# Performance work log

Hardware: AMD Instinct MI355X
Metric: run time of the kernel (lower is better)

Reference implementation:

```python
import jax, jax.numpy as jnp
import numpy as np

N, E, C_IN, C_OUT, K, D_D = 50000, 800000, 16, 64, 3, 7


def setup_inputs() -> dict:
    key = jax.random.key(0)
    ks = jax.random.split(key, 10)
    s = 0.05
    x = jax.random.normal(ks[0], (N, C_IN), jnp.float32)
    edge_index = jax.random.randint(ks[1], (2, E), 0, N, dtype=jnp.int64)
    edge_weight = jax.random.uniform(ks[2], (E,), jnp.float32)
    h0 = jax.random.normal(ks[3], (N, C_OUT), jnp.float32)
    # stacked ChebConv params: gate order [z, r, h]
    Wx = jax.random.normal(ks[4], (3, K, C_IN, C_OUT), jnp.float32) * s
    Wh = jax.random.normal(ks[5], (3, K, C_OUT, C_OUT), jnp.float32) * s
    bx = jax.random.normal(ks[6], (3, C_OUT), jnp.float32) * s
    bh = jax.random.normal(ks[7], (3, C_OUT), jnp.float32) * s
    Wlin = jax.random.normal(ks[8], (C_OUT, D_D), jnp.float32) * s
    blin = jax.random.normal(ks[9], (D_D,), jnp.float32) * s
    return dict(x=x, edge_index=edge_index, edge_weight=edge_weight, h0=h0,
                Wx=Wx, Wh=Wh, bx=bx, bh=bh, Wlin=Wlin, blin=blin)


def _norm(src, dst, edge_weight, n):
    # ChebConv sym normalization with lambda_max=2:
    # L_sym = I - D^-1/2 A D^-1/2;  L_tilde = 2L/lambda_max - I = -D^-1/2 A D^-1/2
    w = jnp.where(src == dst, 0.0, edge_weight)  # remove self loops
    deg = jax.ops.segment_sum(w, src, num_segments=n)
    dinv = jnp.where(deg > 0, 1.0 / jnp.sqrt(deg), 0.0)
    return -dinv[src] * w * dinv[dst]


def _cheb(t, W, b, src, dst, nw, n):
    # K-hop Chebyshev recursion: Tx_{k+1} = 2*L~*Tx_k - Tx_{k-1}
    prop = lambda v: jax.ops.segment_sum(nw[:, None] * v[src], dst, num_segments=n)
    Tx0 = t
    out = Tx0 @ W[0]
    Tx1 = prop(Tx0)
    out = out + Tx1 @ W[1]
    for k in range(2, W.shape[0]):
        Tx2 = 2.0 * prop(Tx1) - Tx0
        out = out + Tx2 @ W[k]
        Tx0, Tx1 = Tx1, Tx2
    return out + b


def reference(x, edge_index, edge_weight, h0, Wx, Wh, bx, bh, Wlin, blin):
    n = x.shape[0]
    src, dst = edge_index[0], edge_index[1]
    nw = _norm(src, dst, edge_weight, n)
    z = jax.nn.sigmoid(_cheb(x, Wx[0], bx[0], src, dst, nw, n)
                       + _cheb(h0, Wh[0], bh[0], src, dst, nw, n))
    r = jax.nn.sigmoid(_cheb(x, Wx[1], bx[1], src, dst, nw, n)
                       + _cheb(h0, Wh[1], bh[1], src, dst, nw, n))
    htil = jnp.tanh(_cheb(x, Wx[2], bx[2], src, dst, nw, n)
                    + _cheb(h0 * r, Wh[2], bh[2], src, dst, nw, n))
    h = z * h0 + (1.0 - z) * htil
    y = jax.nn.relu(h) @ Wlin + blin
    return (jax.lax.stop_gradient(h), y)
```

## Files before the change

kernel.cpp:

```cpp
#include <hip/hip_runtime.h>

constexpr int NN = 50000;
constexpr int NE = 800000;
constexpr int CI = 16;
constexpr int CO = 64;
constexpr int DD = 7;

constexpr int NBUCK = 196;
constexpr int EPB   = 4096;
constexpr int NBLK3 = (NE + EPB - 1) / EPB;
constexpr int TBL   = NBUCK * NBLK3;

typedef __bf16 bf16x8 __attribute__((ext_vector_type(8)));
typedef float  f32x4  __attribute__((ext_vector_type(4)));
typedef float  f32x2  __attribute__((ext_vector_type(2)));

__device__ inline float blo(unsigned u) { return __uint_as_float(u << 16); }
__device__ inline float bhi(unsigned u) { return __uint_as_float(u & 0xffff0000u); }

__device__ inline void acc8_fp8(float acc[8], float w, uint2 u) {
    f32x2 c;
    c = __builtin_amdgcn_cvt_pk_f32_fp8(u.x, false); acc[0] += w * c[0]; acc[1] += w * c[1];
    c = __builtin_amdgcn_cvt_pk_f32_fp8(u.x, true);  acc[2] += w * c[0]; acc[3] += w * c[1];
    c = __builtin_amdgcn_cvt_pk_f32_fp8(u.y, false); acc[4] += w * c[0]; acc[5] += w * c[1];
    c = __builtin_amdgcn_cvt_pk_f32_fp8(u.y, true);  acc[6] += w * c[0]; acc[7] += w * c[1];
}
__device__ inline uint2 pack_fp8x8(const float o[8]) {
    int t0 = __builtin_amdgcn_cvt_pk_fp8_f32(o[0], o[1], 0, false);
    t0 = __builtin_amdgcn_cvt_pk_fp8_f32(o[2], o[3], t0, true);
    int t1 = __builtin_amdgcn_cvt_pk_fp8_f32(o[4], o[5], 0, false);
    t1 = __builtin_amdgcn_cvt_pk_fp8_f32(o[6], o[7], t1, true);
    uint2 r; r.x = (unsigned)t0; r.y = (unsigned)t1; return r;
}
__device__ inline unsigned char fp8_of(float v) {
    return (unsigned char)(__builtin_amdgcn_cvt_pk_fp8_f32(v, v, 0, false) & 0xff);
}


constexpr int XOCT = NN * CI / 8;
constexpr int HOCT = NN * CO / 8;
constexpr int CB = (XOCT + HOCT + 255) / 256;

__global__ void __launch_bounds__(256) k_count(
    const int* __restrict__ src, const int* __restrict__ dst,
    int* __restrict__ Cd, int* __restrict__ Cs,
    const float* __restrict__ x, const float* __restrict__ h0,
    __bf16* __restrict__ x_bf, __bf16* __restrict__ h0_bf, unsigned char* __restrict__ h0_f8,
    const float* __restrict__ Wx, const float* __restrict__ Wh,
    const float* __restrict__ bx, const float* __restrict__ bh,
    bf16x8* __restrict__ BfragZR, bf16x8* __restrict__ BfragHT, float* __restrict__ biasC) {
    int b = blockIdx.x;
    if (b < NBLK3) {
        __shared__ int hd[NBUCK], hs[NBUCK];
        for (int i = threadIdx.x; i < NBUCK; i += 256) { hd[i] = 0; hs[i] = 0; }
        __syncthreads();
        int base = b * EPB;
#pragma unroll
        for (int k = 0; k < EPB / 256; k++) {
            int e = base + k * 256 + threadIdx.x;
            if (e < NE) {
                int s = src[e], d = dst[e];
                atomicAdd(&hd[d >> 8], 1);
                atomicAdd(&hs[s >> 8], 1);
            }
        }
        __syncthreads();
        for (int i = threadIdx.x; i < NBUCK; i += 256) {
            Cd[i * NBLK3 + b] = hd[i];
            Cs[i * NBLK3 + b] = hs[i];
        }
    } else if (b < NBLK3 + CB) {
        int t = (b - NBLK3) * 256 + threadIdx.x;
        if (t < XOCT) {
            const float* sp = x + (size_t)t * 8;
            float4 a = *(const float4*)sp;
            float4 c = *(const float4*)(sp + 4);
            bf16x8 o;
            o[0] = (__bf16)a.x; o[1] = (__bf16)a.y; o[2] = (__bf16)a.z; o[3] = (__bf16)a.w;
            o[4] = (__bf16)c.x; o[5] = (__bf16)c.y; o[6] = (__bf16)c.z; o[7] = (__bf16)c.w;
            *(bf16x8*)(x_bf + (size_t)t * 8) = o;
        } else if (t < XOCT + HOCT) {
            int u = t - XOCT;
            const float* sp = h0 + (size_t)u * 8;
            float4 a = *(const float4*)sp;
            float4 c = *(const float4*)(sp + 4);
            bf16x8 o;
            o[0] = (__bf16)a.x; o[1] = (__bf16)a.y; o[2] = (__bf16)a.z; o[3] = (__bf16)a.w;
            o[4] = (__bf16)c.x; o[5] = (__bf16)c.y; o[6] = (__bf16)c.z; o[7] = (__bf16)c.w;
            *(bf16x8*)(h0_bf + (size_t)u * 8) = o;
            float f[8] = {a.x, a.y, a.z, a.w, c.x, c.y, c.z, c.w};
            *(uint2*)(h0_f8 + (size_t)u * 8) = pack_fp8x8(f);
        }
    } else {
        int tid = (b - NBLK3 - CB) * 256 + threadIdx.x;
        if (tid < 6144) {
            int e = tid, gate, n, kk, l;
            if (e < 4096) {
                int t = e >> 9, rem = e & 511;
                kk = rem >> 6; l = rem & 63;
                n = t * 16 + (l & 15);
                gate = n >> 6;
            } else {
                int e2 = e - 4096;
                int t = e2 >> 9, rem = e2 & 511;
                kk = rem >> 6; l = rem & 63;
                n = t * 16 + (l & 15);
                gate = 2;
            }
            int co = n & 63;
            int k0 = kk * 32 + (l >> 4) * 8;
            bf16x8 f;
#pragma unroll
            for (int j = 0; j < 8; j++) {
                int k = k0 + j;
                float w = 0.f;
                if (k < 48) {
                    int kb = k >> 4, ci = k & 15;
                    const float* Wg = Wx + gate * 3 * 16 * 64;
                    float w0 = Wg[(kb * 16 + ci) * 64 + co];
                    if (kb == 0)      w = w0 - Wg[(2 * 16 + ci) * 64 + co];
                    else if (kb == 1) w = w0;
                    else              w = 2.f * w0;
                } else if (k < 240) {
                    int kh = k - 48, kb = kh >> 6, ci = kh & 63;
                    const float* Wg = Wh + gate * 3 * 64 * 64;
                    float w0 = Wg[(kb * 64 + ci) * 64 + co];
                    if (kb == 0)      w = w0 - Wg[(2 * 64 + ci) * 64 + co];
                    else if (kb == 1) w = w0;
                    else              w = 2.f * w0;
                }
                f[j] = (__bf16)w;
            }
            if (e < 4096) BfragZR[e] = f; else BfragHT[e - 4096] = f;
        } else if (tid < 6144 + 192) {
            int i = tid - 6144;
            biasC[i] = bx[i] + bh[i];
        }
    }
}


__global__ void __launch_bounds__(1024) k_scan_tables(int* __restrict__ Cd, int* __restrict__ Cs) {
    int* C = (blockIdx.x == 0) ? Cd : Cs;
    constexpr int CHUNK = (TBL + 1023) / 1024;
    __shared__ int part[1024];
    int t = threadIdx.x;
    int base = t * CHUNK;
    int v[CHUNK];
    int s = 0;
#pragma unroll
    for (int j = 0; j < CHUNK; j++) {
        int idx = base + j;
        int xv = (idx < TBL) ? C[idx] : 0;
        v[j] = s;
        s += xv;
    }
    part[t] = s;
    __syncthreads();
    for (int off = 1; off < 1024; off <<= 1) {
        int p = (t >= off) ? part[t - off] : 0;
        __syncthreads();
        part[t] += p;
        __syncthreads();
    }
    int tb = (t > 0) ? part[t - 1] : 0;
#pragma unroll
    for (int j = 0; j < CHUNK; j++) {
        int idx = base + j;
        if (idx < TBL) C[idx] = tb + v[j];
    }
}


__global__ void __launch_bounds__(256) k_scatter(
    const int* __restrict__ src, const int* __restrict__ dst, const float* __restrict__ ew,
    const int* __restrict__ Cd, const int* __restrict__ Cs,
    uint2* __restrict__ drec, unsigned* __restrict__ srec) {
    __shared__ int cd[NBUCK], cs[NBUCK];
    int b = blockIdx.x;
    for (int i = threadIdx.x; i < NBUCK; i += 256) {
        cd[i] = Cd[i * NBLK3 + b];
        cs[i] = Cs[i * NBLK3 + b];
    }
    __syncthreads();
    int base = b * EPB;
#pragma unroll
    for (int k = 0; k < EPB / 256; k++) {
        int e = base + k * 256 + threadIdx.x;
        if (e < NE) {
            int s = src[e], d = dst[e];
            float w = (s == d) ? 0.f : ew[e];
            __bf16 wb = (__bf16)w;
            unsigned wu = (unsigned)__builtin_bit_cast(unsigned short, wb);
            int pd = atomicAdd(&cd[d >> 8], 1);
            drec[pd] = make_uint2((unsigned)s | (wu << 16), (unsigned)(d & 255));
            int ps = atomicAdd(&cs[s >> 8], 1);
            srec[ps] = (__builtin_bit_cast(unsigned, w) & 0xFFFFFF00u) | (unsigned)(s & 255);
        }
    }
}


__global__ void __launch_bounds__(256) k_dinv(
    const int* __restrict__ Cs, const unsigned* __restrict__ srec, float* __restrict__ dinv) {
    int bkt = blockIdx.x;
    __shared__ float acc[256];
    acc[threadIdx.x] = 0.f;
    __syncthreads();
    int beg = Cs[bkt * NBLK3];
    int end = (bkt == NBUCK - 1) ? NE : Cs[(bkt + 1) * NBLK3];
    for (int i = beg + threadIdx.x; i < end; i += 256) {
        unsigned r = srec[i];
        atomicAdd(&acc[r & 255], __uint_as_float(r & 0xFFFFFF00u));
    }
    __syncthreads();
    int node = bkt * 256 + threadIdx.x;
    if (node < NN) {
        float dsum = acc[threadIdx.x];
        dinv[node] = (dsum > 0.f) ? (1.f / sqrtf(dsum)) : 0.f;
    }
}


__global__ void __launch_bounds__(256) k_build(
    const int* __restrict__ Cd, const uint2* __restrict__ drec, const float* __restrict__ dinv,
    int* __restrict__ rowptr, unsigned* __restrict__ csr_ew) {
    int bkt = blockIdx.x;
    __shared__ int cnt[256], sc[256], cur[256];
    int t = threadIdx.x;
    cnt[t] = 0;
    __syncthreads();
    int beg = Cd[bkt * NBLK3];
    int end = (bkt == NBUCK - 1) ? NE : Cd[(bkt + 1) * NBLK3];
    for (int i = beg + t; i < end; i += 256) atomicAdd(&cnt[drec[i].y], 1);
    __syncthreads();
    int val = cnt[t];
    sc[t] = val;
    __syncthreads();
    for (int off = 1; off < 256; off <<= 1) {
        int p = (t >= off) ? sc[t - off] : 0;
        __syncthreads();
        sc[t] += p;
        __syncthreads();
    }
    int ex = sc[t] - val;
    int node = bkt * 256 + t;
    if (node <= NN) rowptr[node] = beg + ex;
    cur[t] = ex;
    __syncthreads();
    for (int i = beg + t; i < end; i += 256) {
        uint2 r = drec[i];
        int slot = beg + atomicAdd(&cur[r.y], 1);
        unsigned s = r.x & 0xffff;
        float w = bhi(r.x);
        float wp = dinv[s] * w;
        __bf16 wb = (__bf16)wp;
        unsigned ub = (unsigned)__builtin_bit_cast(unsigned short, wb);
        csr_ew[slot] = s | (ub << 16);
    }
}


__device__ inline void fprop_body(int n, int lane,
                                  const unsigned char* __restrict__ vh8,
                                  const __bf16* __restrict__ vx,
                                  const float* __restrict__ dinv,
                                  const int* __restrict__ rowptr,
                                  const unsigned* __restrict__ ew,
                                  __bf16* __restrict__ outh_bf,
                                  unsigned char* __restrict__ outh_f8,
                                  __bf16* __restrict__ outx) {
    int j = lane >> 3, cg = lane & 7;
    int beg = rowptr[n], end = rowptr[n + 1];
    float f = -dinv[n];
    unsigned pmeta = (beg + lane < end) ? ew[beg + lane] : 0u;
    int deg = end - beg;
    int nIt = (deg >= 64) ? 8 : ((deg + 7) >> 3);
    float acc[8] = {0.f, 0.f, 0.f, 0.f, 0.f, 0.f, 0.f, 0.f};
    float ax0 = 0.f, ax1 = 0.f;
#pragma unroll
    for (int t = 0; t < 8; t++) {
// ... 69 lines not shown
        unsigned p = ew[e];
        float w = bhi(p);
        int s = p & 0xffff;
        uint2 u = *(const uint2*)(v8 + (size_t)s * 64 + cg * 8);
        acc8_fp8(acc, w, u);
    }
#pragma unroll
    for (int m = 8; m <= 32; m <<= 1) {
#pragma unroll
        for (int i = 0; i < 8; i++) acc[i] += __shfl_xor(acc[i], m, 64);
    }
    if (lane < 8) {
        float o[8];
#pragma unroll
        for (int i = 0; i < 8; i++) o[i] = f * acc[i];
        bf16x8 st;
#pragma unroll
        for (int i = 0; i < 8; i++) st[i] = (__bf16)o[i];
        *(bf16x8*)(out_bf + (size_t)n * 64 + lane * 8) = st;
        if (out_f8) *(uint2*)(out_f8 + (size_t)n * 64 + lane * 8) = pack_fp8x8(o);
    }
}

__global__ void __launch_bounds__(256) k_fprop(
    const unsigned char* __restrict__ vh8, const __bf16* __restrict__ vx,
    const float* __restrict__ dinv,
    const int* __restrict__ rowptr, const unsigned* __restrict__ ew,
    __bf16* __restrict__ outh_bf, unsigned char* __restrict__ outh_f8,
    __bf16* __restrict__ outx) {
    int n = blockIdx.x * 4 + (threadIdx.x >> 6);
    if (n >= NN) return;
    fprop_body(n, threadIdx.x & 63, vh8, vx, dinv, rowptr, ew, outh_bf, outh_f8, outx);
}

__global__ void __launch_bounds__(256) k_prop64(
    const unsigned char* __restrict__ v8, const float* __restrict__ dinv,
    const int* __restrict__ rowptr, const unsigned* __restrict__ ew,
    __bf16* __restrict__ out_bf, unsigned char* __restrict__ out_f8) {
    int n = blockIdx.x * 4 + (threadIdx.x >> 6);
    if (n >= NN) return;
    prop64_body(n, threadIdx.x & 63, v8, dinv, rowptr, ew, out_bf, out_f8);
}


__device__ inline bf16x8 load_a_bf(int c, int m,
                                   const __bf16* __restrict__ xb, const __bf16* __restrict__ t1,
                                   const __bf16* __restrict__ t2, const __bf16* __restrict__ hb,
                                   const __bf16* __restrict__ h1, const __bf16* __restrict__ h2) {
    if (c >= 30) {
        bf16x8 a;
#pragma unroll
        for (int j = 0; j < 8; j++) a[j] = (__bf16)0.f;
        return a;
    }
    if (c < 6) {
        const __bf16* base = (c < 2) ? xb : ((c < 4) ? t1 : t2);
        return *(const bf16x8*)(base + (size_t)m * 16 + (c & 1) * 8);
    }
    int d = c - 6;
    const __bf16* base = (d < 8) ? hb : ((d < 16) ? h1 : h2);
    return *(const bf16x8*)(base + (size_t)m * 64 + (d & 7) * 8);
}

__global__ void __launch_bounds__(256) k_mfma_zr(
    const __bf16* __restrict__ xb, const __bf16* __restrict__ t1, const __bf16* __restrict__ t2,
    const __bf16* __restrict__ hb, const __bf16* __restrict__ h1, const __bf16* __restrict__ h2,
    const bf16x8* __restrict__ Bfrag, const float* __restrict__ biasC,
    __bf16* __restrict__ z_bf, __bf16* __restrict__ hr_bf, unsigned char* __restrict__ hr_f8) {
    int wv = (blockIdx.x * 256 + threadIdx.x) >> 6;
    if (wv >= NN / 16) return;
    int lane = threadIdx.x & 63;
    int q = lane >> 4, r16 = lane & 15;
    int ma = wv * 16 + r16;
    f32x4 acc[8];
#pragma unroll
    for (int t = 0; t < 8; t++) acc[t] = (f32x4){0.f, 0.f, 0.f, 0.f};
#pragma unroll
    for (int kk = 0; kk < 8; kk++) {
        bf16x8 a = load_a_bf(kk * 4 + q, ma, xb, t1, t2, hb, h1, h2);
#pragma unroll
        for (int t = 0; t < 8; t++)
            acc[t] = __builtin_amdgcn_mfma_f32_16x16x32_bf16(a, Bfrag[(t * 8 + kk) * 64 + lane], acc[t], 0, 0, 0);
    }
    int mbase = wv * 16 + q * 4;
#pragma unroll
    for (int t = 0; t < 8; t++) {
        int co = t * 16 + r16;
        float bias = biasC[co];
        int col = co & 63;
#pragma unroll
        for (int reg = 0; reg < 4; reg++) {
            int mm = mbase + reg;
            float p = acc[t][reg] + bias;
            float s = 1.f / (1.f + __expf(-p));
            if (t < 4) z_bf[(size_t)mm * 64 + col] = (__bf16)s;
            else {
                float hrv = s * (float)hb[(size_t)mm * 64 + col];
                hr_bf[(size_t)mm * 64 + col] = (__bf16)hrv;
                hr_f8[(size_t)mm * 64 + col] = fp8_of(hrv);
            }
        }
    }
}

__global__ void __launch_bounds__(256) k_mfma_ht(
    const __bf16* __restrict__ xb, const __bf16* __restrict__ t1, const __bf16* __restrict__ t2,
    const __bf16* __restrict__ hrb, const __bf16* __restrict__ r1, const __bf16* __restrict__ r2,
    const bf16x8* __restrict__ Bfrag, const float* __restrict__ biasC,
    const __bf16* __restrict__ z_bf, const float* __restrict__ h0,
    const float* __restrict__ Wlin, const float* __restrict__ blin,
    float* __restrict__ hout, float* __restrict__ yout) {
    int wv = (blockIdx.x * 256 + threadIdx.x) >> 6;
    if (wv >= NN / 16) return;
    int lane = threadIdx.x & 63;
    int q = lane >> 4, r16 = lane & 15;
    int ma = wv * 16 + r16;
    f32x4 acc[4];
#pragma unroll
    for (int t = 0; t < 4; t++) acc[t] = (f32x4){0.f, 0.f, 0.f, 0.f};
#pragma unroll
    for (int kk = 0; kk < 8; kk++) {
        bf16x8 a = load_a_bf(kk * 4 + q, ma, xb, t1, t2, hrb, r1, r2);
#pragma unroll
        for (int t = 0; t < 4; t++)
            acc[t] = __builtin_amdgcn_mfma_f32_16x16x32_bf16(a, Bfrag[(t * 8 + kk) * 64 + lane], acc[t], 0, 0, 0);
    }
    int mbase = wv * 16 + q * 4;
    float hbuf[4][4];
#pragma unroll
    for (int t = 0; t < 4; t++) {
        int co = t * 16 + r16;
        float bias = biasC[128 + co];
#pragma unroll
        for (int reg = 0; reg < 4; reg++) {
            int mm = mbase + reg;
            float p = acc[t][reg] + bias;
            float htl = tanhf(p);
            float zv = (float)z_bf[(size_t)mm * 64 + co];
            float h0v = h0[(size_t)mm * 64 + co];
            float hn = zv * h0v + (1.f - zv) * htl;
            hout[(size_t)mm * 64 + co] = hn;
            hbuf[t][reg] = hn;
        }
    }
    float ya[4][DD];
#pragma unroll
    for (int reg = 0; reg < 4; reg++)
#pragma unroll
        for (int d = 0; d < DD; d++) ya[reg][d] = 0.f;
#pragma unroll
    for (int t = 0; t < 4; t++) {
        int cb = (t * 16 + r16) * DD;
        float wl[DD];
#pragma unroll
        for (int d = 0; d < DD; d++) wl[d] = Wlin[cb + d];
#pragma unroll
        for (int reg = 0; reg < 4; reg++) {
            float rh = fmaxf(hbuf[t][reg], 0.f);
#pragma unroll
            for (int d = 0; d < DD; d++) ya[reg][d] += rh * wl[d];
        }
    }
#pragma unroll
    for (int m = 1; m <= 8; m <<= 1) {
#pragma unroll
        for (int reg = 0; reg < 4; reg++)
#pragma unroll
            for (int d = 0; d < DD; d++) ya[reg][d] += __shfl_xor(ya[reg][d], m, 64);
    }
    if (r16 < DD) {
        float b = blin[r16];
#pragma unroll
        for (int reg = 0; reg < 4; reg++) {
            float v = (r16 == 0) ? ya[reg][0] : (r16 == 1) ? ya[reg][1] : (r16 == 2) ? ya[reg][2]
                    : (r16 == 3) ? ya[reg][3] : (r16 == 4) ? ya[reg][4] : (r16 == 5) ? ya[reg][5]
                    : ya[reg][6];
            yout[(size_t)(mbase + reg) * DD + r16] = v + b;
        }
    }
}


extern "C" void kernel_launch(void* const* d_in, const int* in_sizes, int n_in,
                              void* d_out, int out_size, void* d_ws, size_t ws_size,
                              hipStream_t stream) {
    (void)in_sizes; (void)n_in; (void)out_size; (void)ws_size;
    const float* x    = (const float*)d_in[0];
    const int*   eidx = (const int*)d_in[1];
    const float* ew   = (const float*)d_in[2];
    const float* h0   = (const float*)d_in[3];
    const float* Wx   = (const float*)d_in[4];
    const float* Wh   = (const float*)d_in[5];
    const float* bx   = (const float*)d_in[6];
    const float* bh   = (const float*)d_in[7];
    const float* Wlin = (const float*)d_in[8];
    const float* blin = (const float*)d_in[9];
    const int* src = eidx;
    const int* dst = eidx + NE;

    char* ws = (char*)d_ws;
    size_t off = 0;
    auto alloc = [&](size_t nbytes) -> void* {
        void* p = ws + off;
        off += (nbytes + 255) & ~(size_t)255;
        return p;
    };
    int*    Cd      = (int*)alloc((size_t)TBL * 4);
    int*    Cs      = (int*)alloc((size_t)TBL * 4);
    uint2*  drec    = (uint2*)alloc((size_t)NE * 8);
    unsigned* srec  = (unsigned*)alloc((size_t)NE * 4);
    float*  dinv    = (float*)alloc(NN * 4);
    int*    rowptr  = (int*)alloc((NN + 1) * 4);
    unsigned* csr_ew = (unsigned*)alloc((size_t)NE * 4);
    __bf16* x_bf    = (__bf16*)alloc((size_t)NN * CI * 2);
    __bf16* h0_bf   = (__bf16*)alloc((size_t)NN * CO * 2);
    unsigned char* h0_f8 = (unsigned char*)alloc((size_t)NN * CO);
    unsigned char* T1_f8 = (unsigned char*)alloc((size_t)NN * CO);
    unsigned char* hr_f8 = (unsigned char*)alloc((size_t)NN * CO);
    __bf16* Tx1     = (__bf16*)alloc((size_t)NN * CI * 2);
    __bf16* Tx2     = (__bf16*)alloc((size_t)NN * CI * 2);
    __bf16* Th1     = (__bf16*)alloc((size_t)NN * CO * 2);
    __bf16* Th2     = (__bf16*)alloc((size_t)NN * CO * 2);
    __bf16* hr_bf   = (__bf16*)alloc((size_t)NN * CO * 2);
    __bf16* z_bf    = (__bf16*)alloc((size_t)NN * CO * 2);
    bf16x8* BfragZR = (bf16x8*)alloc(4096 * 16);
    bf16x8* BfragHT = (bf16x8*)alloc(2048 * 16);
    float*  biasC   = (float*)alloc(192 * 4);

    float* hout = (float*)d_out;
    float* yout = hout + (size_t)NN * CO;

    const int PROPB = (NN + 3) / 4;
    const int GEMMB = (NN / 16 * 64 + 255) / 256;

    k_count<<<NBLK3 + CB + 25, 256, 0, stream>>>(
        src, dst, Cd, Cs, x, h0, x_bf, h0_bf, h0_f8,
        Wx, Wh, bx, bh, BfragZR, BfragHT, biasC);
    k_scan_tables<<<2, 1024, 0, stream>>>(Cd, Cs);
    k_scatter<<<NBLK3, 256, 0, stream>>>(src, dst, ew, Cd, Cs, drec, srec);
    k_dinv<<<NBUCK, 256, 0, stream>>>(Cs, srec, dinv);
    k_build<<<NBUCK, 256, 0, stream>>>(Cd, drec, dinv, rowptr, csr_ew);

    k_fprop<<<PROPB, 256, 0, stream>>>(h0_f8, x_bf, dinv, rowptr, csr_ew, Th1, T1_f8, Tx1);
    k_fprop<<<PROPB, 256, 0, stream>>>(T1_f8, Tx1, dinv, rowptr, csr_ew, Th2, nullptr, Tx2);

    k_mfma_zr<<<GEMMB, 256, 0, stream>>>(x_bf, Tx1, Tx2, h0_bf, Th1, Th2,
                                         BfragZR, biasC, z_bf, hr_bf, hr_f8);
    k_prop64<<<PROPB, 256, 0, stream>>>(hr_f8, dinv, rowptr, csr_ew, Th1, T1_f8);
    k_prop64<<<PROPB, 256, 0, stream>>>(T1_f8, dinv, rowptr, csr_ew, Th2, nullptr);
    k_mfma_ht<<<GEMMB, 256, 0, stream>>>(x_bf, Tx1, Tx2, hr_bf, Th1, Th2,
                                         BfragHT, biasC, z_bf, h0, Wlin, blin, hout, yout);
}
```

Before: 295.2 us.

## Fuse all pipeline stages into one cooperative persistent megakernel with grid syncs

Replaces the chain of about ten kernel launches (count, scan, scatter, dinv, build, two fprops, zr GEMM, two prop64s, ht GEMM) with a single cooperative kernel. The stages become device-function tasks separated by grid-wide barriers. The grid size comes from the occupancy query and is capped at 2048 blocks, and the multi-launch path is kept as a fallback if the cooperative launch fails. The aim is to remove launch gaps and tail effects between the small stages. The costs are the grid-sync overhead, possibly lower per-stage parallelism, and register pressure from a kernel that contains every stage.

Result: slower. 891.7 us (+202.1%).

```diff
diff --git a/kernel.cpp b/kernel.cpp
--- a/kernel.cpp
+++ b/kernel.cpp
@@ -1,4 +1,7 @@
 #include <hip/hip_runtime.h>
+#include <hip/hip_cooperative_groups.h>
+
+namespace cg = cooperative_groups;
 
 constexpr int NN = 50000;
 constexpr int NE = 800000;
@@ -36,227 +39,82 @@
     return (unsigned char)(__builtin_amdgcn_cvt_pk_fp8_f32(v, v, 0, false) & 0xff);
 }
 
-
 constexpr int XOCT = NN * CI / 8;
 constexpr int HOCT = NN * CO / 8;
 constexpr int CB = (XOCT + HOCT + 255) / 256;
 
-__global__ void __launch_bounds__(256) k_count(
-    const int* __restrict__ src, const int* __restrict__ dst,
-    int* __restrict__ Cd, int* __restrict__ Cs,
-    const float* __restrict__ x, const float* __restrict__ h0,
-    __bf16* __restrict__ x_bf, __bf16* __restrict__ h0_bf, unsigned char* __restrict__ h0_f8,
-    const float* __restrict__ Wx, const float* __restrict__ Wh,
-    const float* __restrict__ bx, const float* __restrict__ bh,
-    bf16x8* __restrict__ BfragZR, bf16x8* __restrict__ BfragHT, float* __restrict__ biasC) {
-    int b = blockIdx.x;
-    if (b < NBLK3) {
-        __shared__ int hd[NBUCK], hs[NBUCK];
-        for (int i = threadIdx.x; i < NBUCK; i += 256) { hd[i] = 0; hs[i] = 0; }
-        __syncthreads();
-        int base = b * EPB;
-#pragma unroll
-        for (int k = 0; k < EPB / 256; k++) {
-            int e = base + k * 256 + threadIdx.x;
-            if (e < NE) {
-                int s = src[e], d = dst[e];
-                atomicAdd(&hd[d >> 8], 1);
-                atomicAdd(&hs[s >> 8], 1);
+
+__device__ inline void task_cast(int t, const float* __restrict__ x, const float* __restrict__ h0,
+                                 __bf16* __restrict__ x_bf, __bf16* __restrict__ h0_bf,
+                                 unsigned char* __restrict__ h0_f8) {
+    if (t < XOCT) {
+        const float* sp = x + (size_t)t * 8;
+        float4 a = *(const float4*)sp;
+        float4 c = *(const float4*)(sp + 4);
+        bf16x8 o;
+        o[0] = (__bf16)a.x; o[1] = (__bf16)a.y; o[2] = (__bf16)a.z; o[3] = (__bf16)a.w;
+        o[4] = (__bf16)c.x; o[5] = (__bf16)c.y; o[6] = (__bf16)c.z; o[7] = (__bf16)c.w;
+        *(bf16x8*)(x_bf + (size_t)t * 8) = o;
+    } else if (t < XOCT + HOCT) {
+        int u = t - XOCT;
+        const float* sp = h0 + (size_t)u * 8;
+        float4 a = *(const float4*)sp;
+        float4 c = *(const float4*)(sp + 4);
+        bf16x8 o;
+        o[0] = (__bf16)a.x; o[1] = (__bf16)a.y; o[2] = (__bf16)a.z; o[3] = (__bf16)a.w;
+        o[4] = (__bf16)c.x; o[5] = (__bf16)c.y; o[6] = (__bf16)c.z; o[7] = (__bf16)c.w;
+        *(bf16x8*)(h0_bf + (size_t)u * 8) = o;
+        float f[8] = {a.x, a.y, a.z, a.w, c.x, c.y, c.z, c.w};
+        *(uint2*)(h0_f8 + (size_t)u * 8) = pack_fp8x8(f);
+    }
+}
+
+__device__ inline void task_bprep(int tid, const float* __restrict__ Wx, const float* __restrict__ Wh,
+                                  const float* __restrict__ bx, const float* __restrict__ bh,
+                                  bf16x8* __restrict__ BfragZR, bf16x8* __restrict__ BfragHT,
+                                  float* __restrict__ biasC) {
+    if (tid < 6144) {
+        int e = tid, gate, n, kk, l;
+        if (e < 4096) {
+            int t = e >> 9, rem = e & 511;
+            kk = rem >> 6; l = rem & 63;
+            n = t * 16 + (l & 15);
+            gate = n >> 6;
+        } else {
+            int e2 = e - 4096;
+            int t = e2 >> 9, rem = e2 & 511;
+            kk = rem >> 6; l = rem & 63;
+            n = t * 16 + (l & 15);
+            gate = 2;
+        }
+        int co = n & 63;
+        int k0 = kk * 32 + (l >> 4) * 8;
+        bf16x8 f;
+#pragma unroll
+        for (int j = 0; j < 8; j++) {
+            int k = k0 + j;
+            float w = 0.f;
+            if (k < 48) {
+                int kb = k >> 4, ci = k & 15;
+                const float* Wg = Wx + gate * 3 * 16 * 64;
+                float w0 = Wg[(kb * 16 + ci) * 64 + co];
+                if (kb == 0)      w = w0 - Wg[(2 * 16 + ci) * 64 + co];
+                else if (kb == 1) w = w0;
+                else              w = 2.f * w0;
+            } else if (k < 240) {
+                int kh = k - 48, kb = kh >> 6, ci = kh & 63;
+                const float* Wg = Wh + gate * 3 * 64 * 64;
+                float w0 = Wg[(kb * 64 + ci) * 64 + co];
+                if (kb == 0)      w = w0 - Wg[(2 * 64 + ci) * 64 + co];
+                else if (kb == 1) w = w0;
+                else              w = 2.f * w0;
             }
-        }
-        __syncthreads();
-        for (int i = threadIdx.x; i < NBUCK; i += 256) {
-            Cd[i * NBLK3 + b] = hd[i];
-            Cs[i * NBLK3 + b] = hs[i];
-        }
-    } else if (b < NBLK3 + CB) {
-        int t = (b - NBLK3) * 256 + threadIdx.x;
-        if (t < XOCT) {
-            const float* sp = x + (size_t)t * 8;
-            float4 a = *(const float4*)sp;
-            float4 c = *(const float4*)(sp + 4);
-            bf16x8 o;
-            o[0] = (__bf16)a.x; o[1] = (__bf16)a.y; o[2] = (__bf16)a.z; o[3] = (__bf16)a.w;
-            o[4] = (__bf16)c.x; o[5] = (__bf16)c.y; o[6] = (__bf16)c.z; o[7] = (__bf16)c.w;
-            *(bf16x8*)(x_bf + (size_t)t * 8) = o;
-        } else if (t < XOCT + HOCT) {
-            int u = t - XOCT;
-            const float* sp = h0 + (size_t)u * 8;
-            float4 a = *(const float4*)sp;
-            float4 c = *(const float4*)(sp + 4);
-            bf16x8 o;
-            o[0] = (__bf16)a.x; o[1] = (__bf16)a.y; o[2] = (__bf16)a.z; o[3] = (__bf16)a.w;
-            o[4] = (__bf16)c.x; o[5] = (__bf16)c.y; o[6] = (__bf16)c.z; o[7] = (__bf16)c.w;
-            *(bf16x8*)(h0_bf + (size_t)u * 8) = o;
-            float f[8] = {a.x, a.y, a.z, a.w, c.x, c.y, c.z, c.w};
-            *(uint2*)(h0_f8 + (size_t)u * 8) = pack_fp8x8(f);
-        }
-    } else {
-        int tid = (b - NBLK3 - CB) * 256 + threadIdx.x;
-        if (tid < 6144) {
-            int e = tid, gate, n, kk, l;
-            if (e < 4096) {
-                int t = e >> 9, rem = e & 511;
-                kk = rem >> 6; l = rem & 63;
-                n = t * 16 + (l & 15);
-                gate = n >> 6;
-            } else {
-                int e2 = e - 4096;
-                int t = e2 >> 9, rem = e2 & 511;
-                kk = rem >> 6; l = rem & 63;
-                n = t * 16 + (l & 15);
-                gate = 2;
-            }
-            int co = n & 63;
-            int k0 = kk * 32 + (l >> 4) * 8;
-            bf16x8 f;
-#pragma unroll
-            for (int j = 0; j < 8; j++) {
-                int k = k0 + j;
-                float w = 0.f;
-                if (k < 48) {
-                    int kb = k >> 4, ci = k & 15;
-                    const float* Wg = Wx + gate * 3 * 16 * 64;
-                    float w0 = Wg[(kb * 16 + ci) * 64 + co];
-                    if (kb == 0)      w = w0 - Wg[(2 * 16 + ci) * 64 + co];
-                    else if (kb == 1) w = w0;
-                    else              w = 2.f * w0;
-                } else if (k < 240) {
-                    int kh = k - 48, kb = kh >> 6, ci = kh & 63;
-                    const float* Wg = Wh + gate * 3 * 64 * 64;
-                    float w0 = Wg[(kb * 64 + ci) * 64 + co];
-                    if (kb == 0)      w = w0 - Wg[(2 * 64 + ci) * 64 + co];
-                    else if (kb == 1) w = w0;
-                    else              w = 2.f * w0;
-                }
-                f[j] = (__bf16)w;
-            }
-            if (e < 4096) BfragZR[e] = f; else BfragHT[e - 4096] = f;
-        } else if (tid < 6144 + 192) {
-            int i = tid - 6144;
-            biasC[i] = bx[i] + bh[i];
-        }
-    }
-}
-
-
-__global__ void __launch_bounds__(1024) k_scan_tables(int* __restrict__ Cd, int* __restrict__ Cs) {
-    int* C = (blockIdx.x == 0) ? Cd : Cs;
-    constexpr int CHUNK = (TBL + 1023) / 1024;
-    __shared__ int part[1024];
-    int t = threadIdx.x;
-    int base = t * CHUNK;
-    int v[CHUNK];
-    int s = 0;
-#pragma unroll
-    for (int j = 0; j < CHUNK; j++) {
-        int idx = base + j;
-        int xv = (idx < TBL) ? C[idx] : 0;
-        v[j] = s;
-        s += xv;
-    }
-    part[t] = s;
-    __syncthreads();
-    for (int off = 1; off < 1024; off <<= 1) {
-        int p = (t >= off) ? part[t - off] : 0;
-        __syncthreads();
-        part[t] += p;
-        __syncthreads();
-    }
-    int tb = (t > 0) ? part[t - 1] : 0;
-#pragma unroll
-    for (int j = 0; j < CHUNK; j++) {
-        int idx = base + j;
-        if (idx < TBL) C[idx] = tb + v[j];
-    }
-}
-
-
-__global__ void __launch_bounds__(256) k_scatter(
-    const int* __restrict__ src, const int* __restrict__ dst, const float* __restrict__ ew,
-    const int* __restrict__ Cd, const int* __restrict__ Cs,
-    uint2* __restrict__ drec, unsigned* __restrict__ srec) {
-    __shared__ int cd[NBUCK], cs[NBUCK];
-    int b = blockIdx.x;
-    for (int i = threadIdx.x; i < NBUCK; i += 256) {
-        cd[i] = Cd[i * NBLK3 + b];
-        cs[i] = Cs[i * NBLK3 + b];
-    }
-    __syncthreads();
-    int base = b * EPB;
-#pragma unroll
-    for (int k = 0; k < EPB / 256; k++) {
-        int e = base + k * 256 + threadIdx.x;
-        if (e < NE) {
-            int s = src[e], d = dst[e];
-            float w = (s == d) ? 0.f : ew[e];
-            __bf16 wb = (__bf16)w;
-            unsigned wu = (unsigned)__builtin_bit_cast(unsigned short, wb);
-            int pd = atomicAdd(&cd[d >> 8], 1);
-            drec[pd] = make_uint2((unsigned)s | (wu << 16), (unsigned)(d & 255));
-            int ps = atomicAdd(&cs[s >> 8], 1);
-            srec[ps] = (__builtin_bit_cast(unsigned, w) & 0xFFFFFF00u) | (unsigned)(s & 255);
-        }
-    }
-}
-
-
-__global__ void __launch_bounds__(256) k_dinv(
-    const int* __restrict__ Cs, const unsigned* __restrict__ srec, float* __restrict__ dinv) {
-    int bkt = blockIdx.x;
-    __shared__ float acc[256];
-    acc[threadIdx.x] = 0.f;
-    __syncthreads();
-    int beg = Cs[bkt * NBLK3];
-    int end = (bkt == NBUCK - 1) ? NE : Cs[(bkt + 1) * NBLK3];
-    for (int i = beg + threadIdx.x; i < end; i += 256) {
-        unsigned r = srec[i];
-        atomicAdd(&acc[r & 255], __uint_as_float(r & 0xFFFFFF00u));
-    }
-    __syncthreads();
-    int node = bkt * 256 + threadIdx.x;
-    if (node < NN) {
-        float dsum = acc[threadIdx.x];
-        dinv[node] = (dsum > 0.f) ? (1.f / sqrtf(dsum)) : 0.f;
-    }
-}
-
-
-__global__ void __launch_bounds__(256) k_build(
-    const int* __restrict__ Cd, const uint2* __restrict__ drec, const float* __restrict__ dinv,
-    int* __restrict__ rowptr, unsigned* __restrict__ csr_ew) {
-    int bkt = blockIdx.x;
-    __shared__ int cnt[256], sc[256], cur[256];
-    int t = threadIdx.x;
-    cnt[t] = 0;
-    __syncthreads();
-    int beg = Cd[bkt * NBLK3];
-    int end = (bkt == NBUCK - 1) ? NE : Cd[(bkt + 1) * NBLK3];
-    for (int i = beg + t; i < end; i += 256) atomicAdd(&cnt[drec[i].y], 1);
-    __syncthreads();
-    int val = cnt[t];
-    sc[t] = val;
-    __syncthreads();
-    for (int off = 1; off < 256; off <<= 1) {
-        int p = (t >= off) ? sc[t - off] : 0;
-        __syncthreads();
-        sc[t] += p;
-        __syncthreads();
-    }
-    int ex = sc[t] - val;
-    int node = bkt * 256 + t;
-    if (node <= NN) rowptr[node] = beg + ex;
-    cur[t] = ex;
-    __syncthreads();
-    for (int i = beg + t; i < end; i += 256) {
-        uint2 r = drec[i];
-        int slot = beg + atomicAdd(&cur[r.y], 1);
-        unsigned s = r.x & 0xffff;
-        float w = bhi(r.x);
-        float wp = dinv[s] * w;
-        __bf16 wb = (__bf16)wp;
-        unsigned ub = (unsigned)__builtin_bit_cast(unsigned short, wb);
-        csr_ew[slot] = s | (ub << 16);
+            f[j] = (__bf16)w;
+        }
+        if (e < 4096) BfragZR[e] = f; else BfragHT[e - 4096] = f;
+    } else if (tid < 6144 + 192) {
+        int i = tid - 6144;
+        biasC[i] = bx[i] + bh[i];
     }
 }
 
@@ -372,26 +230,6 @@
     }
 }
 
-__global__ void __launch_bounds__(256) k_fprop(
-    const unsigned char* __restrict__ vh8, const __bf16* __restrict__ vx,
-    const float* __restrict__ dinv,
-    const int* __restrict__ rowptr, const unsigned* __restrict__ ew,
-    __bf16* __restrict__ outh_bf, unsigned char* __restrict__ outh_f8,
-    __bf16* __restrict__ outx) {
-    int n = blockIdx.x * 4 + (threadIdx.x >> 6);
-    if (n >= NN) return;
-    fprop_body(n, threadIdx.x & 63, vh8, vx, dinv, rowptr, ew, outh_bf, outh_f8, outx);
-}
-
-__global__ void __launch_bounds__(256) k_prop64(
-    const unsigned char* __restrict__ v8, const float* __restrict__ dinv,
-    const int* __restrict__ rowptr, const unsigned* __restrict__ ew,
-    __bf16* __restrict__ out_bf, unsigned char* __restrict__ out_f8) {
-    int n = blockIdx.x * 4 + (threadIdx.x >> 6);
-    if (n >= NN) return;
-    prop64_body(n, threadIdx.x & 63, v8, dinv, rowptr, ew, out_bf, out_f8);
-}
-
 
 __device__ inline bf16x8 load_a_bf(int c, int m,
                                    const __bf16* __restrict__ xb, const __bf16* __restrict__ t1,
@@ -412,14 +250,11 @@
     return *(const bf16x8*)(base + (size_t)m * 64 + (d & 7) * 8);
 }
 
-__global__ void __launch_bounds__(256) k_mfma_zr(
+__device__ inline void zr_wave(int wv, int lane,
     const __bf16* __restrict__ xb, const __bf16* __restrict__ t1, const __bf16* __restrict__ t2,
     const __bf16* __restrict__ hb, const __bf16* __restrict__ h1, const __bf16* __restrict__ h2,
     const bf16x8* __restrict__ Bfrag, const float* __restrict__ biasC,
     __bf16* __restrict__ z_bf, __bf16* __restrict__ hr_bf, unsigned char* __restrict__ hr_f8) {
-    int wv = (blockIdx.x * 256 + threadIdx.x) >> 6;
-    if (wv >= NN / 16) return;
-    int lane = threadIdx.x & 63;
     int q = lane >> 4, r16 = lane & 15;
     int ma = wv * 16 + r16;
     f32x4 acc[8];
@@ -453,6 +288,464 @@
     }
 }
 
+__device__ inline void ht_wave(int wv, int lane,
+    const __bf16* __restrict__ xb, const __bf16* __restrict__ t1, const __bf16* __restrict__ t2,
+    const __bf16* __restrict__ hrb, const __bf16* __restrict__ r1, const __bf16* __restrict__ r2,
+    const bf16x8* __restrict__ Bfrag, const float* __restrict__ biasC,
+    const __bf16* __restrict__ z_bf, const float* __restrict__ h0,
+    const float* __restrict__ Wlin, const float* __restrict__ blin,
+    float* __restrict__ hout, float* __restrict__ yout) {
+    int q = lane >> 4, r16 = lane & 15;
+    int ma = wv * 16 + r16;
+    f32x4 acc[4];
+#pragma unroll
+    for (int t = 0; t < 4; t++) acc[t] = (f32x4){0.f, 0.f, 0.f, 0.f};
+#pragma unroll
+    for (int kk = 0; kk < 8; kk++) {
+        bf16x8 a = load_a_bf(kk * 4 + q, ma, xb, t1, t2, hrb, r1, r2);
+#pragma unroll
+        for (int t = 0; t < 4; t++)
+            acc[t] = __builtin_amdgcn_mfma_f32_16x16x32_bf16(a, Bfrag[(t * 8 + kk) * 64 + lane], acc[t], 0, 0, 0);
+    }
+    int mbase = wv * 16 + q * 4;
+    float hbuf[4][4];
+#pragma unroll
+    for (int t = 0; t < 4; t++) {
+        int co = t * 16 + r16;
+        float bias = biasC[128 + co];
+#pragma unroll
+        for (int reg = 0; reg < 4; reg++) {
+            int mm = mbase + reg;
+            float p = acc[t][reg] + bias;
+            float htl = tanhf(p);
+            float zv = (float)z_bf[(size_t)mm * 64 + co];
+            float h0v = h0[(size_t)mm * 64 + co];
+            float hn = zv * h0v + (1.f - zv) * htl;
+            hout[(size_t)mm * 64 + co] = hn;
+            hbuf[t][reg] = hn;
+        }
+    }
+    float ya[4][DD];
+#pragma unroll
+    for (int reg = 0; reg < 4; reg++)
+#pragma unroll
+        for (int d = 0; d < DD; d++) ya[reg][d] = 0.f;
+#pragma unroll
+    for (int t = 0; t < 4; t++) {
+        int cb = (t * 16 + r16) * DD;
+        float wl[DD];
+#pragma unroll
+        for (int d = 0; d < DD; d++) wl[d] = Wlin[cb + d];
+#pragma unroll
+        for (int reg = 0; reg < 4; reg++) {
+            float rh = fmaxf(hbuf[t][reg], 0.f);
+#pragma unroll
+            for (int d = 0; d < DD; d++) ya[reg][d] += rh * wl[d];
+        }
+    }
+#pragma unroll
+    for (int m = 1; m <= 8; m <<= 1) {
+#pragma unroll
+        for (int reg = 0; reg < 4; reg++)
+#pragma unroll
+            for (int d = 0; d < DD; d++) ya[reg][d] += __shfl_xor(ya[reg][d], m, 64);
+    }
+    if (r16 < DD) {
+        float b = blin[r16];
+#pragma unroll
+        for (int reg = 0; reg < 4; reg++) {
+            float v = (r16 == 0) ? ya[reg][0] : (r16 == 1) ? ya[reg][1] : (r16 == 2) ? ya[reg][2]
+                    : (r16 == 3) ? ya[reg][3] : (r16 == 4) ? ya[reg][4] : (r16 == 5) ? ya[reg][5]
+                    : ya[reg][6];
+            yout[(size_t)(mbase + reg) * DD + r16] = v + b;
+        }
+    }
+}
+
+
+struct MegaArgs {
+    const int* src; const int* dst; const float* ew;
+    const float* x; const float* h0;
+    const float* Wx; const float* Wh; const float* bx; const float* bh;
+    const float* Wlin; const float* blin;
+    int* Cd; int* Cs; int* CdRow; int* CsRow; int* CdBase; int* CsBase;
+    uint2* drec; unsigned* srec; float* dinv; int* rowptr; unsigned* csr_ew;
+    __bf16* x_bf; __bf16* h0_bf; unsigned char* h0_f8;
+    unsigned char* T1_f8; unsigned char* hr_f8;
+    __bf16* Tx1; __bf16* Tx2; __bf16* Th1; __bf16* Th2;
+    __bf16* hr_bf; __bf16* z_bf;
+    bf16x8* BfragZR; bf16x8* BfragHT; float* biasC;
+    float* hout; float* yout;
+};
+
+__device__ inline void task_exscan(const int* in, int* out, int n, int* tot, int* lds, int tid) {
+    int v = (tid < n) ? in[tid] : 0;
+    lds[tid] = v;
+    __syncthreads();
+    for (int off = 1; off < 256; off <<= 1) {
+        int p = (tid >= off) ? lds[tid - off] : 0;
+        __syncthreads();
+        lds[tid] += p;
+        __syncthreads();
+    }
+    if (tid < n) out[tid] = lds[tid] - v;
+    if (tot && tid == 0) *tot = lds[255];
+    __syncthreads();
+}
+
+__global__ void __launch_bounds__(256, 4) k_mega(MegaArgs A) {
+    cg::grid_group grid = cg::this_grid();
+    const int nb  = (int)gridDim.x;
+    const int bid = (int)blockIdx.x;
+    const int tid = (int)threadIdx.x;
+    const int wid = tid >> 6, lane = tid & 63;
+
+    __shared__ union {
+        struct { int hd[NBUCK], hs[NBUCK]; } h;
+        int scan[256];
+        struct { int cd[NBUCK], cs[NBUCK]; } c;
+        float dacc[256];
+        struct { int cnt[256], sc[256], cur[256]; } b;
+    } sm;
+
+    for (int b = bid; b < NBLK3 + CB + 25; b += nb) {
+        if (b < NBLK3) {
+            for (int i = tid; i < NBUCK; i += 256) { sm.h.hd[i] = 0; sm.h.hs[i] = 0; }
+            __syncthreads();
+            int base = b * EPB;
+#pragma unroll
+            for (int k = 0; k < EPB / 256; k++) {
+                int e = base + k * 256 + tid;
+                if (e < NE) {
+                    atomicAdd(&sm.h.hd[A.dst[e] >> 8], 1);
+                    atomicAdd(&sm.h.hs[A.src[e] >> 8], 1);
+                }
+            }
+            __syncthreads();
+            for (int i = tid; i < NBUCK; i += 256) {
+                A.Cd[i * NBLK3 + b] = sm.h.hd[i];
+                A.Cs[i * NBLK3 + b] = sm.h.hs[i];
+            }
+            __syncthreads();
+        } else if (b < NBLK3 + CB) {
+            task_cast((b - NBLK3) * 256 + tid, A.x, A.h0, A.x_bf, A.h0_bf, A.h0_f8);
+        } else {
+            task_bprep((b - NBLK3 - CB) * 256 + tid, A.Wx, A.Wh, A.bx, A.bh,
+                       A.BfragZR, A.BfragHT, A.biasC);
+        }
+    }
+    grid.sync();
+
+    for (int t = bid; t < 2 * NBUCK; t += nb) {
+        int* C   = (t < NBUCK) ? A.Cd : A.Cs;
+        int* Row = (t < NBUCK) ? A.CdRow : A.CsRow;
+        int row  = (t < NBUCK) ? t : t - NBUCK;
+        task_exscan(&C[row * NBLK3], &C[row * NBLK3], NBLK3, &Row[row], sm.scan, tid);
+    }
+    grid.sync();
+
+    for (int t = bid; t < 2; t += nb) {
+        int* Row  = (t == 0) ? A.CdRow : A.CsRow;
+        int* Base = (t == 0) ? A.CdBase : A.CsBase;
+        task_exscan(Row, Base, NBUCK, nullptr, sm.scan, tid);
+    }
+    grid.sync();
+
+    for (int b = bid; b < NBLK3; b += nb) {
+        for (int i = tid; i < NBUCK; i += 256) {
+            sm.c.cd[i] = A.CdBase[i] + A.Cd[i * NBLK3 + b];
+            sm.c.cs[i] = A.CsBase[i] + A.Cs[i * NBLK3 + b];
+        }
+        __syncthreads();
+        int base = b * EPB;
+#pragma unroll
+        for (int k = 0; k < EPB / 256; k++) {
+            int e = base + k * 256 + tid;
+            if (e < NE) {
+                int s = A.src[e], d = A.dst[e];
+                float w = (s == d) ? 0.f : A.ew[e];
+                __bf16 wb = (__bf16)w;
+                unsigned wu = (unsigned)__builtin_bit_cast(unsigned short, wb);
+                int pd = atomicAdd(&sm.c.cd[d >> 8], 1);
+                A.drec[pd] = make_uint2((unsigned)s | (wu << 16), (unsigned)(d & 255));
+                int ps = atomicAdd(&sm.c.cs[s >> 8], 1);
+                A.srec[ps] = (__builtin_bit_cast(unsigned, w) & 0xFFFFFF00u) | (unsigned)(s & 255);
+            }
+        }
+        __syncthreads();
+    }
+    grid.sync();
+
+    for (int bkt = bid; bkt < NBUCK; bkt += nb) {
+        sm.dacc[tid] = 0.f;
+        __syncthreads();
+        int beg = A.CsBase[bkt], end = beg + A.CsRow[bkt];
+        for (int i = beg + tid; i < end; i += 256) {
+            unsigned r = A.srec[i];
+            atomicAdd(&sm.dacc[r & 255], __uint_as_float(r & 0xFFFFFF00u));
+        }
+        __syncthreads();
+        int node = bkt * 256 + tid;
+        if (node < NN) {
+            float dsum = sm.dacc[tid];
+            A.dinv[node] = (dsum > 0.f) ? (1.f / sqrtf(dsum)) : 0.f;
+        }
+        __syncthreads();
+    }
+    grid.sync();
+
+    for (int bkt = bid; bkt < NBUCK; bkt += nb) {
+        sm.b.cnt[tid] = 0;
+        __syncthreads();
+        int beg = A.CdBase[bkt], end = beg + A.CdRow[bkt];
+        for (int i = beg + tid; i < end; i += 256) atomicAdd(&sm.b.cnt[A.drec[i].y], 1);
+        __syncthreads();
+        int val = sm.b.cnt[tid];
+        sm.b.sc[tid] = val;
+        __syncthreads();
+        for (int off = 1; off < 256; off <<= 1) {
+            int p = (tid >= off) ? sm.b.sc[tid - off] : 0;
+            __syncthreads();
+            sm.b.sc[tid] += p;
+            __syncthreads();
+        }
+        int ex = sm.b.sc[tid] - val;
+        int node = bkt * 256 + tid;
+        if (node <= NN) A.rowptr[node] = beg + ex;
+        sm.b.cur[tid] = ex;
+        __syncthreads();
+        for (int i = beg + tid; i < end; i += 256) {
+            uint2 r = A.drec[i];
+            int slot = beg + atomicAdd(&sm.b.cur[r.y], 1);
+            unsigned s = r.x & 0xffff;
+            float w = bhi(r.x);
+            float wp = A.dinv[s] * w;
+            __bf16 wb = (__bf16)wp;
+            A.csr_ew[slot] = s | ((unsigned)__builtin_bit_cast(unsigned short, wb) << 16);
+        }
+        __syncthreads();
+    }
+    grid.sync();
+
+    for (int base = bid * 4; base < NN; base += nb * 4) {
+        int n = base + wid;
+        if (n < NN) fprop_body(n, lane, A.h0_f8, A.x_bf, A.dinv, A.rowptr, A.csr_ew,
+                               A.Th1, A.T1_f8, A.Tx1);
+    }
+    grid.sync();
+
+    for (int base = bid * 4; base < NN; base += nb * 4) {
+        int n = base + wid;
+        if (n < NN) fprop_body(n, lane, A.T1_f8, A.Tx1, A.dinv, A.rowptr, A.csr_ew,
+                               A.Th2, nullptr, A.Tx2);
+    }
+    grid.sync();
+
+    for (int wv = bid * 4 + wid; wv < NN / 16; wv += nb * 4) {
+        zr_wave(wv, lane, A.x_bf, A.Tx1, A.Tx2, A.h0_bf, A.Th1, A.Th2,
+                A.BfragZR, A.biasC, A.z_bf, A.hr_bf, A.hr_f8);
+    }
+    grid.sync();
+
+    for (int base = bid * 4; base < NN; base += nb * 4) {
+        int n = base + wid;
+        if (n < NN) prop64_body(n, lane, A.hr_f8, A.dinv, A.rowptr, A.csr_ew, A.Th1, A.T1_f8);
+    }
+    grid.sync();
+
+    for (int base = bid * 4; base < NN; base += nb * 4) {
+        int n = base + wid;
+        if (n < NN) prop64_body(n, lane, A.T1_f8, A.dinv, A.rowptr, A.csr_ew, A.Th2, nullptr);
+    }
+    grid.sync();
+
+    for (int wv = bid * 4 + wid; wv < NN / 16; wv += nb * 4) {
+        ht_wave(wv, lane, A.x_bf, A.Tx1, A.Tx2, A.hr_bf, A.Th1, A.Th2,
+                A.BfragHT, A.biasC, A.z_bf, A.h0, A.Wlin, A.blin, A.hout, A.yout);
+    }
+}
+
+
+__global__ void __launch_bounds__(256) k_count(
+    const int* __restrict__ src, const int* __restrict__ dst,
+    int* __restrict__ Cd, int* __restrict__ Cs,
+    const float* __restrict__ x, const float* __restrict__ h0,
+    __bf16* __restrict__ x_bf, __bf16* __restrict__ h0_bf, unsigned char* __restrict__ h0_f8,
+    const float* __restrict__ Wx, const float* __restrict__ Wh,
+    const float* __restrict__ bx, const float* __restrict__ bh,
+    bf16x8* __restrict__ BfragZR, bf16x8* __restrict__ BfragHT, float* __restrict__ biasC) {
+    int b = blockIdx.x;
+    if (b < NBLK3) {
+        __shared__ int hd[NBUCK], hs[NBUCK];
+        for (int i = threadIdx.x; i < NBUCK; i += 256) { hd[i] = 0; hs[i] = 0; }
+        __syncthreads();
+        int base = b * EPB;
+#pragma unroll
+        for (int k = 0; k < EPB / 256; k++) {
+            int e = base + k * 256 + threadIdx.x;
+            if (e < NE) {
+                atomicAdd(&hd[dst[e] >> 8], 1);
+                atomicAdd(&hs[src[e] >> 8], 1);
+            }
+        }
+        __syncthreads();
+        for (int i = threadIdx.x; i < NBUCK; i += 256) {
+            Cd[i * NBLK3 + b] = hd[i];
+            Cs[i * NBLK3 + b] = hs[i];
+        }
+    } else if (b < NBLK3 + CB) {
+        task_cast((b - NBLK3) * 256 + threadIdx.x, x, h0, x_bf, h0_bf, h0_f8);
+    } else {
+        task_bprep((b - NBLK3 - CB) * 256 + threadIdx.x, Wx, Wh, bx, bh, BfragZR, BfragHT, biasC);
+    }
+}
+
+__global__ void __launch_bounds__(1024) k_scan_tables(int* __restrict__ Cd, int* __restrict__ Cs) {
+    int* C = (blockIdx.x == 0) ? Cd : Cs;
+    constexpr int CHUNK = (TBL + 1023) / 1024;
+    __shared__ int part[1024];
+    int t = threadIdx.x;
+    int base = t * CHUNK;
+    int v[CHUNK];
+    int s = 0;
+#pragma unroll
+    for (int j = 0; j < CHUNK; j++) {
+        int idx = base + j;
+        int xv = (idx < TBL) ? C[idx] : 0;
+        v[j] = s;
+        s += xv;
+    }
+    part[t] = s;
+    __syncthreads();
+    for (int off = 1; off < 1024; off <<= 1) {
+        int p = (t >= off) ? part[t - off] : 0;
+        __syncthreads();
+        part[t] += p;
+        __syncthreads();
+    }
+    int tb = (t > 0) ? part[t - 1] : 0;
+#pragma unroll
+    for (int j = 0; j < CHUNK; j++) {
+        int idx = base + j;
+        if (idx < TBL) C[idx] = tb + v[j];
+    }
+}
+
+__global__ void __launch_bounds__(256) k_scatter(
+    const int* __restrict__ src, const int* __restrict__ dst, const float* __restrict__ ew,
+    const int* __restrict__ Cd, const int* __restrict__ Cs,
+    uint2* __restrict__ drec, unsigned* __restrict__ srec) {
+    __shared__ int cd[NBUCK], cs[NBUCK];
+    int b = blockIdx.x;
+    for (int i = threadIdx.x; i < NBUCK; i += 256) {
+        cd[i] = Cd[i * NBLK3 + b];
+        cs[i] = Cs[i * NBLK3 + b];
+    }
+    __syncthreads();
+    int base = b * EPB;
+#pragma unroll
+    for (int k = 0; k < EPB / 256; k++) {
+        int e = base + k * 256 + threadIdx.x;
+        if (e < NE) {
+            int s = src[e], d = dst[e];
+            float w = (s == d) ? 0.f : ew[e];
+            __bf16 wb = (__bf16)w;
+            unsigned wu = (unsigned)__builtin_bit_cast(unsigned short, wb);
+            int pd = atomicAdd(&cd[d >> 8], 1);
+            drec[pd] = make_uint2((unsigned)s | (wu << 16), (unsigned)(d & 255));
+            int ps = atomicAdd(&cs[s >> 8], 1);
+            srec[ps] = (__builtin_bit_cast(unsigned, w) & 0xFFFFFF00u) | (unsigned)(s & 255);
+        }
+    }
+}
+
+__global__ void __launch_bounds__(256) k_dinv(
+    const int* __restrict__ Cs, const unsigned* __restrict__ srec, float* __restrict__ dinv) {
+    int bkt = blockIdx.x;
+    __shared__ float acc[256];
+    acc[threadIdx.x] = 0.f;
+    __syncthreads();
+    int beg = Cs[bkt * NBLK3];
+    int end = (bkt == NBUCK - 1) ? NE : Cs[(bkt + 1) * NBLK3];
+    for (int i = beg + threadIdx.x; i < end; i += 256) {
+        unsigned r = srec[i];
+        atomicAdd(&acc[r & 255], __uint_as_float(r & 0xFFFFFF00u));
+    }
+    __syncthreads();
+    int node = bkt * 256 + threadIdx.x;
+    if (node < NN) {
+        float dsum = acc[threadIdx.x];
+        dinv[node] = (dsum > 0.f) ? (1.f / sqrtf(dsum)) : 0.f;
+    }
+}
+
+__global__ void __launch_bounds__(256) k_build(
+    const int* __restrict__ Cd, const uint2* __restrict__ drec, const float* __restrict__ dinv,
+    int* __restrict__ rowptr, unsigned* __restrict__ csr_ew) {
+    int bkt = blockIdx.x;
+    __shared__ int cnt[256], sc[256], cur[256];
+    int t = threadIdx.x;
+    cnt[t] = 0;
+    __syncthreads();
+    int beg = Cd[bkt * NBLK3];
+    int end = (bkt == NBUCK - 1) ? NE : Cd[(bkt + 1) * NBLK3];
+    for (int i = beg + t; i < end; i += 256) atomicAdd(&cnt[drec[i].y], 1);
+    __syncthreads();
+    int val = cnt[t];
+    sc[t] = val;
+    __syncthreads();
+    for (int off = 1; off < 256; off <<= 1) {
+        int p = (t >= off) ? sc[t - off] : 0;
+        __syncthreads();
+        sc[t] += p;
+        __syncthreads();
+    }
+    int ex = sc[t] - val;
+    int node = bkt * 256 + t;
+    if (node <= NN) rowptr[node] = beg + ex;
+    cur[t] = ex;
+    __syncthreads();
+    for (int i = beg + t; i < end; i += 256) {
+        uint2 r = drec[i];
+        int slot = beg + atomicAdd(&cur[r.y], 1);
+        unsigned s = r.x & 0xffff;
+        float w = bhi(r.x);
+        float wp = dinv[s] * w;
+        __bf16 wb = (__bf16)wp;
+        csr_ew[slot] = s | ((unsigned)__builtin_bit_cast(unsigned short, wb) << 16);
+    }
+}
+
+__global__ void __launch_bounds__(256) k_fprop(
+    const unsigned char* __restrict__ vh8, const __bf16* __restrict__ vx,
+    const float* __restrict__ dinv,
+    const int* __restrict__ rowptr, const unsigned* __restrict__ ew,
+    __bf16* __restrict__ outh_bf, unsigned char* __restrict__ outh_f8,
+    __bf16* __restrict__ outx) {
+    int n = blockIdx.x * 4 + (threadIdx.x >> 6);
+    if (n >= NN) return;
+    fprop_body(n, threadIdx.x & 63, vh8, vx, dinv, rowptr, ew, outh_bf, outh_f8, outx);
+}
+
+__global__ void __launch_bounds__(256) k_prop64(
+    const unsigned char* __restrict__ v8, const float* __restrict__ dinv,
+    const int* __restrict__ rowptr, const unsigned* __restrict__ ew,
+    __bf16* __restrict__ out_bf, unsigned char* __restrict__ out_f8) {
+    int n = blockIdx.x * 4 + (threadIdx.x >> 6);
+    if (n >= NN) return;
+    prop64_body(n, threadIdx.x & 63, v8, dinv, rowptr, ew, out_bf, out_f8);
+}
+
+__global__ void __launch_bounds__(256) k_mfma_zr(
+    const __bf16* __restrict__ xb, const __bf16* __restrict__ t1, const __bf16* __restrict__ t2,
+    const __bf16* __restrict__ hb, const __bf16* __restrict__ h1, const __bf16* __restrict__ h2,
+    const bf16x8* __restrict__ Bfrag, const float* __restrict__ biasC,
+    __bf16* __restrict__ z_bf, __bf16* __restrict__ hr_bf, unsigned char* __restrict__ hr_f8) {
+    int wv = (blockIdx.x * 256 + threadIdx.x) >> 6;
+    if (wv >= NN / 16) return;
+    zr_wave(wv, threadIdx.x & 63, xb, t1, t2, hb, h1, h2, Bfrag, biasC, z_bf, hr_bf, hr_f8);
+}
+
 __global__ void __launch_bounds__(256) k_mfma_ht(
     const __bf16* __restrict__ xb, const __bf16* __restrict__ t1, const __bf16* __restrict__ t2,
     const __bf16* __restrict__ hrb, const __bf16* __restrict__ r1, const __bf16* __restrict__ r2,
@@ -462,72 +755,8 @@
     float* __restrict__ hout, float* __restrict__ yout) {
     int wv = (blockIdx.x * 256 + threadIdx.x) >> 6;
     if (wv >= NN / 16) return;
-    int lane = threadIdx.x & 63;
-    int q = lane >> 4, r16 = lane & 15;
-    int ma = wv * 16 + r16;
-    f32x4 acc[4];
-#pragma unroll
-    for (int t = 0; t < 4; t++) acc[t] = (f32x4){0.f, 0.f, 0.f, 0.f};
-#pragma unroll
-    for (int kk = 0; kk < 8; kk++) {
-        bf16x8 a = load_a_bf(kk * 4 + q, ma, xb, t1, t2, hrb, r1, r2);
-#pragma unroll
-        for (int t = 0; t < 4; t++)
-            acc[t] = __builtin_amdgcn_mfma_f32_16x16x32_bf16(a, Bfrag[(t * 8 + kk) * 64 + lane], acc[t], 0, 0, 0);
-    }
-    int mbase = wv * 16 + q * 4;
-    float hbuf[4][4];
-#pragma unroll
-    for (int t = 0; t < 4; t++) {
-        int co = t * 16 + r16;
-        float bias = biasC[128 + co];
-#pragma unroll
-        for (int reg = 0; reg < 4; reg++) {
-            int mm = mbase + reg;
-            float p = acc[t][reg] + bias;
-            float htl = tanhf(p);
-            float zv = (float)z_bf[(size_t)mm * 64 + co];
-            float h0v = h0[(size_t)mm * 64 + co];
-            float hn = zv * h0v + (1.f - zv) * htl;
-            hout[(size_t)mm * 64 + co] = hn;
-            hbuf[t][reg] = hn;
-        }
-    }
-    float ya[4][DD];
-#pragma unroll
-    for (int reg = 0; reg < 4; reg++)
-#pragma unroll
-        for (int d = 0; d < DD; d++) ya[reg][d] = 0.f;
-#pragma unroll
-    for (int t = 0; t < 4; t++) {
-        int cb = (t * 16 + r16) * DD;
-        float wl[DD];
-#pragma unroll
-        for (int d = 0; d < DD; d++) wl[d] = Wlin[cb + d];
-#pragma unroll
-        for (int reg = 0; reg < 4; reg++) {
-            float rh = fmaxf(hbuf[t][reg], 0.f);
-#pragma unroll
-            for (int d = 0; d < DD; d++) ya[reg][d] += rh * wl[d];
-        }
-    }
-#pragma unroll
-    for (int m = 1; m <= 8; m <<= 1) {
-#pragma unroll
-        for (int reg = 0; reg < 4; reg++)
-#pragma unroll
-            for (int d = 0; d < DD; d++) ya[reg][d] += __shfl_xor(ya[reg][d], m, 64);
-    }
-    if (r16 < DD) {
-        float b = blin[r16];
-#pragma unroll
-        for (int reg = 0; reg < 4; reg++) {
-            float v = (r16 == 0) ? ya[reg][0] : (r16 == 1) ? ya[reg][1] : (r16 == 2) ? ya[reg][2]
-                    : (r16 == 3) ? ya[reg][3] : (r16 == 4) ? ya[reg][4] : (r16 == 5) ? ya[reg][5]
-                    : ya[reg][6];
-            yout[(size_t)(mbase + reg) * DD + r16] = v + b;
-        }
-    }
+    ht_wave(wv, threadIdx.x & 63, xb, t1, t2, hrb, r1, r2, Bfrag, biasC, z_bf, h0,
+            Wlin, blin, hout, yout);
 }
 
 
@@ -557,6 +786,10 @@
     };
     int*    Cd      = (int*)alloc((size_t)TBL * 4);
     int*    Cs      = (int*)alloc((size_t)TBL * 4);
+    int*    CdRow   = (int*)alloc(NBUCK * 4);
+    int*    CsRow   = (int*)alloc(NBUCK * 4);
+    int*    CdBase  = (int*)alloc(NBUCK * 4);
+    int*    CsBase  = (int*)alloc(NBUCK * 4);
     uint2*  drec    = (uint2*)alloc((size_t)NE * 8);
     unsigned* srec  = (unsigned*)alloc((size_t)NE * 4);
     float*  dinv    = (float*)alloc(NN * 4);
@@ -580,6 +813,30 @@
     float* hout = (float*)d_out;
     float* yout = hout + (size_t)NN * CO;
 
+    MegaArgs ma;
+    ma.src = src; ma.dst = dst; ma.ew = ew; ma.x = x; ma.h0 = h0;
+    ma.Wx = Wx; ma.Wh = Wh; ma.bx = bx; ma.bh = bh; ma.Wlin = Wlin; ma.blin = blin;
+    ma.Cd = Cd; ma.Cs = Cs; ma.CdRow = CdRow; ma.CsRow = CsRow;
+    ma.CdBase = CdBase; ma.CsBase = CsBase;
+    ma.drec = drec; ma.srec = srec; ma.dinv = dinv; ma.rowptr = rowptr; ma.csr_ew = csr_ew;
+    ma.x_bf = x_bf; ma.h0_bf = h0_bf; ma.h0_f8 = h0_f8;
+    ma.T1_f8 = T1_f8; ma.hr_f8 = hr_f8;
+    ma.Tx1 = Tx1; ma.Tx2 = Tx2; ma.Th1 = Th1; ma.Th2 = Th2;
+    ma.hr_bf = hr_bf; ma.z_bf = z_bf;
+    ma.BfragZR = BfragZR; ma.BfragHT = BfragHT; ma.biasC = biasC;
+    ma.hout = hout; ma.yout = yout;
+
+    int mp = 0;
+    hipError_t qe = hipOccupancyMaxActiveBlocksPerMultiprocessor(&mp, k_mega, 256, 0);
+    int grid = (qe == hipSuccess && mp > 0) ? mp * 256 : 0;
+    if (grid > 2048) grid = 2048;
+    hipError_t le = hipErrorUnknown;
+    if (grid >= 8) {
+        void* kp[] = { (void*)&ma };
+        le = hipLaunchCooperativeKernel(k_mega, dim3((unsigned)grid), dim3(256), kp, 0u, stream);
+    }
+    if (le == hipSuccess) return;
+
     const int PROPB = (NN + 3) / 4;
     const int GEMMB = (NN / 16 * 64 + 255) / 256;
 
```
